# Kernel tuning notes

Measured on AMD Instinct MI355X. Metric: run time of the kernel, lower is better.

Reference implementation:

```python
import jax, jax.numpy as jnp
import numpy as np

B, T, D, H, WIN, G = 2, 2048, 768, 12, 16, 32
HD = D // H            # 64
K = 2 * WIN + 1        # local kernel size = 33


def setup_inputs() -> dict:
    key = jax.random.key(0)
    ks = jax.random.split(key, 5)
    s = 1.0 / np.sqrt(D).astype(np.float32)
    x = jax.random.normal(ks[0], (B, T, D), jnp.float32)
    # first G tokens of every batch are global (matches original's nonzero(global_mask[b]))
    global_mask = jnp.zeros((B, T), jnp.int32).at[:, :G].set(1)
    Wq = jax.random.normal(ks[1], (D, D), jnp.float32) * s
    Wk = jax.random.normal(ks[2], (D, D), jnp.float32) * s
    Wv = jax.random.normal(ks[3], (D, D), jnp.float32) * s
    Wo = jax.random.normal(ks[4], (D, D), jnp.float32) * s
    bq = jnp.zeros((D,), jnp.float32)
    bk = jnp.zeros((D,), jnp.float32)
    bv = jnp.zeros((D,), jnp.float32)
    bo = jnp.zeros((D,), jnp.float32)
    return {"x": x, "global_mask": global_mask, "Wq": Wq, "bq": bq,
            "Wk": Wk, "bk": bk, "Wv": Wv, "bv": bv, "Wo": Wo, "bo": bo}


def reference(x, global_mask, Wq, bq, Wk, bk, Wv, bv, Wo, bo):
    def split_heads(y):
        return y.reshape(B, T, H, HD).transpose(0, 2, 1, 3)  # [B,H,T,HD]

    q = split_heads(x @ Wq + bq)
    k = split_heads(x @ Wk + bk)
    v = split_heads(x @ Wv + bv)

    scale = 1.0 / np.sqrt(HD).astype(np.float32)

    offs = jnp.arange(-WIN, WIN + 1)
    idx = jnp.arange(T)[:, None] + offs[None, :]          # [T,K]
    valid = (idx >= 0) & (idx < T)                        # [T,K]
    idxc = jnp.clip(idx, 0, T - 1)

    k_loc = k[:, :, idxc]                                 # [B,H,T,K,HD]
    s_loc = jnp.einsum('bhtd,bhtkd->bhtk', q, k_loc) * scale
    s_loc = jnp.where(valid, s_loc, -jnp.inf)             # out-of-range excluded from softmax

    # global tokens (same positions for every batch by construction)
    g_idx = jnp.nonzero(global_mask[0], size=G)[0]        # [G]
    k_g = k[:, :, g_idx]                                  # [B,H,G,HD]
    v_g = v[:, :, g_idx]
    s_g = jnp.einsum('bhtd,bhgd->bhtg', q, k_g) * scale   # [B,H,T,G]

    # joint softmax over [local window, global tokens] (globals in window are double-counted,
    # exactly as in the original torch.cat([local_s, g_score]))
    attn = jax.nn.softmax(jnp.concatenate([s_loc, s_g], axis=-1), axis=-1)
    a_loc = jnp.where(valid, attn[..., :K], 0.0)          # [B,H,T,K]
    a_g = attn[..., K:]                                   # [B,H,T,G]

    v_loc = v[:, :, idxc]                                 # [B,H,T,K,HD]
    ctx = (jnp.einsum('bhtk,bhtkd->bhtd', a_loc, v_loc)
           + jnp.einsum('bhtg,bhgd->bhtd', a_g, v_g))     # [B,H,T,HD]

    out = ctx.transpose(0, 2, 1, 3).reshape(B, T, D) @ Wo + bo

    # dense attention map: scatter local band (add; invalid entries are 0),
    # then overwrite global columns (matches original write order)
    rows = jnp.arange(T)[:, None]                         # [T,1]
    full_attn = jnp.zeros((B, H, T, T), jnp.float32)
    full_attn = full_attn.at[:, :, rows, idxc].add(a_loc)
    full_attn = full_attn.at[:, :, :, g_idx].set(a_g)
    return out, full_attn
```

## Files before the change

kernel.cpp:

```cpp
#include <hip/hip_runtime.h>

typedef unsigned short u16;
typedef __attribute__((ext_vector_type(4))) u16 u16x4;
typedef __attribute__((ext_vector_type(8))) u16 u16x8;
typedef __attribute__((ext_vector_type(8))) short bf16x8;
typedef __attribute__((ext_vector_type(4))) float f32x4;

#define BB 2
#define TT 2048
#define DD 768
#define NH 12
#define HDIM 64
#define NQKV 2304
#define MM 4096

__device__ __forceinline__ u16 f2bf(float f) {
  unsigned u = __float_as_uint(f);
  u += 0x7fffu + ((u >> 16) & 1u);
  return (u16)(u >> 16);
}
__device__ __forceinline__ float bf2f(u16 s) {
  return __uint_as_float(((unsigned)s) << 16);
}
__device__ __forceinline__ void async_load16(const void* g, void* l) {
  __builtin_amdgcn_global_load_lds((const __attribute__((address_space(1))) void*)g,
                                   (__attribute__((address_space(3))) void*)l, 16, 0, 0);
}

__global__ __launch_bounds__(256) void prep_all(const float* __restrict__ x,
                                                const float* __restrict__ Wq, const float* __restrict__ Wk,
                                                const float* __restrict__ Wv, const float* __restrict__ Wo,
                                                const int* __restrict__ gm,
                                                const float* __restrict__ bq, const float* __restrict__ bk,
                                                const float* __restrict__ bv,
                                                u16* __restrict__ xb, u16* __restrict__ wqkvT,
                                                u16* __restrict__ woT,
                                                int* __restrict__ gidx, float* __restrict__ biasqkv) {
  __shared__ float tile[32][33];
  const int bid = blockIdx.x;
  const int tid = threadIdx.x;
  if (bid < 3072) {
    int i = bid * 256 + tid;
    float4 v = ((const float4*)x)[i];
    u16x4 o = { f2bf(v.x), f2bf(v.y), f2bf(v.z), f2bf(v.w) };
    ((u16x4*)xb)[i] = o;
  } else if (bid < 5376) {
    int r = bid - 3072;
    int z = r / 576; r %= 576;
    int kx = r % 24, ny = r / 24;
    const float* W = (z == 0) ? Wq : (z == 1) ? Wk : (z == 2) ? Wv : Wo;
    u16* dst = (z < 3) ? (wqkvT + (size_t)z * DD * DD) : woT;
    int k0 = kx * 32, n0 = ny * 32;
    int tx = tid & 31, ty = tid >> 5;
#pragma unroll
    for (int j = 0; j < 4; ++j)
      tile[ty + j * 8][tx] = W[(size_t)(k0 + ty + j * 8) * DD + n0 + tx];
    __syncthreads();
#pragma unroll
    for (int j = 0; j < 4; ++j)
      dst[(size_t)(n0 + ty + j * 8) * DD + k0 + tx] = f2bf(tile[tx][ty + j * 8]);
  } else {
    for (int n = tid; n < NQKV; n += 256)
      biasqkv[n] = (n < 768) ? bq[n] : (n < 1536) ? bk[n - 768] : bv[n - 1536];
    if (tid < 64) {
      int lane = tid;
      if (lane < 32) gidx[lane] = 0;
      int base = 0;
      for (int c0 = 0; c0 < TT; c0 += 64) {
        int mval = gm[c0 + lane];
        unsigned long long bal = __ballot(mval != 0);
        int pre = __popcll(bal & ((1ull << lane) - 1ull));
        if (mval && (base + pre) < 32) gidx[base + pre] = c0 + lane;
        base += __popcll(bal);
        if (base >= 32) break;
      }
    }
  }
}

__global__ __launch_bounds__(256) void gemm_qkv(const u16* __restrict__ A, const u16* __restrict__ BT,
                                                const float* __restrict__ bias, u16* __restrict__ C,
                                                int Ndim, int Kd) {
  __shared__ __attribute__((aligned(16))) u16 As[128 * 64];
  __shared__ __attribute__((aligned(16))) u16 Bs[128 * 64];
  const int tid = threadIdx.x;
  const int wave = tid >> 6, lane = tid & 63;
  const int m0 = blockIdx.x * 128, n0 = blockIdx.y * 128;
  const int wm = (wave & 1) << 6, wn = (wave >> 1) << 6;
  const int lr = lane & 15, lk = lane >> 4;
  const int srow_b = lane >> 3;
  const int scol = (lane & 7) * 8;

  f32x4 acc[4][4] = {};

  const int kIters = Kd >> 6;
  for (int kt = 0; kt < kIters; ++kt) {
#pragma unroll
    for (int cc = 0; cc < 4; ++cc) {
      int c = wave * 4 + cc;
      int srow = c * 8 + srow_b;
      async_load16(A + (size_t)(m0 + srow) * Kd + (kt << 6) + scol, (void*)(As + c * 512));
      async_load16(BT + (size_t)(n0 + srow) * Kd + (kt << 6) + scol, (void*)(Bs + c * 512));
    }
    __syncthreads();
#pragma unroll
    for (int kc = 0; kc < 2; ++kc) {
      bf16x8 af[4], bfr[4];
#pragma unroll
      for (int i = 0; i < 4; ++i)
        af[i] = *(const bf16x8*)(As + (wm + i * 16 + lr) * 64 + kc * 32 + lk * 8);
#pragma unroll
      for (int j = 0; j < 4; ++j)
        bfr[j] = *(const bf16x8*)(Bs + (wn + j * 16 + lr) * 64 + kc * 32 + lk * 8);
#pragma unroll
      for (int i = 0; i < 4; ++i)
#pragma unroll
        for (int j = 0; j < 4; ++j)
          acc[i][j] = __builtin_amdgcn_mfma_f32_16x16x32_bf16(af[i], bfr[j], acc[i][j], 0, 0, 0);
    }
    __syncthreads();
  }

#pragma unroll
  for (int i = 0; i < 4; ++i) {
    const int row = m0 + wm + i * 16 + lk * 4;
#pragma unroll
    for (int j = 0; j < 4; ++j) {
      const int col = n0 + wn + j * 16 + lr;
      const float bs = bias[col];
#pragma unroll
      for (int r = 0; r < 4; ++r)
        C[(size_t)(row + r) * Ndim + col] = f2bf(acc[i][j][r] + bs);
    }
  }
}

__global__ __launch_bounds__(256) void attn_kernel(const u16* __restrict__ qb,
                                                   const int* __restrict__ gidx,
                                                   u16* __restrict__ ctxb,
                                                   float* __restrict__ probsG) {
  __shared__ __attribute__((aligned(16))) u16 Kl[96 * 72];
  __shared__ __attribute__((aligned(16))) u16 Kg[32 * 72];
  __shared__ __attribute__((aligned(16))) u16 Vl[96 * 72];
  __shared__ __attribute__((aligned(16))) u16 Vg[32 * 72];
  __shared__ __attribute__((aligned(16))) float probs[64 * 68];

  const int tid = threadIdx.x;
  const int blk = blockIdx.x;
  const int chunk = blk & 31;
  const int h = (blk >> 5) % NH;
  const int b = blk / 384;
  const int t0 = chunk << 6;

  {
    const int r = tid >> 3;
    const int c8 = (tid & 7) << 3;
#pragma unroll
    for (int it = 0; it < 3; ++it) {
      int rr = it * 32 + r;
      int t = t0 - 16 + rr;
      t = t < 0 ? 0 : (t > TT - 1 ? TT - 1 : t);
      const u16* src = qb + (size_t)(b * TT + t) * NQKV + h * HDIM + c8;
      *(u16x8*)(Kl + rr * 72 + c8) = *(const u16x8*)(src + 768);
      *(u16x8*)(Vl + rr * 72 + c8) = *(const u16x8*)(src + 1536);
    }
    {
      int t = gidx[r];
      const u16* src = qb + (size_t)(b * TT + t) * NQKV + h * HDIM + c8;
      *(u16x8*)(Kg + r * 72 + c8) = *(const u16x8*)(src + 768);
      *(u16x8*)(Vg + r * 72 + c8) = *(const u16x8*)(src + 1536);
    }
  }
  __syncthreads();

  const int tl = tid >> 2, sub = tid & 3;
  const int t = t0 + tl;
  const u16* qp = qb + (size_t)(b * TT + t) * NQKV + h * HDIM;
  u16x8 qpk[8];
#pragma unroll
  for (int i = 0; i < 8; ++i) qpk[i] = *(const u16x8*)(qp + i * 8);

  float sc[17];
  float mmax = -__builtin_inff();
#pragma unroll
  for (int i = 0; i < 17; ++i) {
    const int s = sub + (i << 2);
    const u16* kp;
    bool valid;
    if (s < 33) { kp = Kl + (tl + s) * 72; int j = t - 16 + s; valid = (j >= 0) && (j < TT); }
    else if (s < 65) { kp = Kg + (s - 33) * 72; valid = true; }
    else { kp = Kg; valid = false; }
    float d = 0.f;
#pragma unroll
    for (int i2 = 0; i2 < 8; ++i2) {
      u16x8 kv = *(const u16x8*)(kp + i2 * 8);
      u16x8 qq = qpk[i2];
#pragma unroll
      for (int e = 0; e < 8; ++e) d += bf2f(qq[e]) * bf2f(kv[e]);
    }
    sc[i] = valid ? d * 0.125f : -__builtin_inff();
    mmax = fmaxf(mmax, sc[i]);
  }
  mmax = fmaxf(mmax, __shfl_xor(mmax, 1));
  mmax = fmaxf(mmax, __shfl_xor(mmax, 2));
  float sum = 0.f;
#pragma unroll
  for (int i = 0; i < 17; ++i) { sc[i] = __expf(sc[i] - mmax); sum += sc[i]; }
  sum += __shfl_xor(sum, 1);
  sum += __shfl_xor(sum, 2);
  const float inv = 1.0f / sum;
#pragma unroll
  for (int i = 0; i < 17; ++i) {
    const int s = sub + (i << 2);
    sc[i] *= inv;
    if (s < 65) probs[tl * 68 + s] = sc[i];
  }
  __syncthreads();

  float cacc[16];
#pragma unroll
  for (int i = 0; i < 16; ++i) cacc[i] = 0.f;
#pragma unroll 1
  for (int k = 0; k < 65; ++k) {
    const float pv = probs[tl * 68 + k];
    const u16* vp = (k < 33) ? (Vl + (tl + k) * 72) : (Vg + (k - 33) * 72);
    const u16* vq = vp + (sub << 4);
    u16x8 v0 = *(const u16x8*)(vq);
    u16x8 v1 = *(const u16x8*)(vq + 8);
#pragma unroll
    for (int e = 0; e < 8; ++e) { cacc[e] += pv * bf2f(v0[e]); cacc[8 + e] += pv * bf2f(v1[e]); }
  }
  {
    u16x8 cb0, cb1;
#pragma unroll
    for (int e = 0; e < 8; ++e) { cb0[e] = f2bf(cacc[e]); cb1[e] = f2bf(cacc[8 + e]); }
    u16* dst = ctxb + (size_t)(b * TT + t) * DD + h * HDIM + (sub << 4);
    *(u16x8*)dst = cb0;
    *(u16x8*)(dst + 8) = cb1;
  }

  {
    float4* dst = (float4*)(probsG + ((size_t)(b * NH + h) * TT + t0) * 68);
    const float4* srcp = (const float4*)probs;
#pragma unroll 1
    for (int i = tid; i < 1088; i += 256) dst[i] = srcp[i];
  }
}

#define G2_BLOCKS 384
__global__ __launch_bounds__(256) void tail_k(const u16* __restrict__ ctxb, const u16* __restrict__ woT,
                                              const float* __restrict__ bo, float* __restrict__ out,
                                              const float* __restrict__ probsG, const int* __restrict__ gidx,
                                              float* __restrict__ fattn) {
  __shared__ __attribute__((aligned(16))) u16 sA[64 * 64];
  __shared__ __attribute__((aligned(16))) u16 sB[128 * 64];
  const int tid = threadIdx.x;
  const int bid = blockIdx.x;

  if (bid < G2_BLOCKS) {
    const int wave = tid >> 6, lane = tid & 63;
    const int m0 = (bid & 63) * 64, n0 = (bid >> 6) * 128;
    const int wn = wave << 5;
    const int lr = lane & 15, lk = lane >> 4;
    const int srow_b = lane >> 3;
    const int scol = (lane & 7) * 8;

    f32x4 acc[4][2] = {};
    for (int kt = 0; kt < DD / 64; ++kt) {
#pragma unroll
      for (int cc = 0; cc < 2; ++cc) {
        int c = wave * 2 + cc;
        int srow = c * 8 + srow_b;
        async_load16(ctxb + (size_t)(m0 + srow) * DD + (kt << 6) + scol, (void*)(sA + c * 512));
      }
#pragma unroll
      for (int cc = 0; cc < 4; ++cc) {
        int c = wave * 4 + cc;
        int srow = c * 8 + srow_b;
        async_load16(woT + (size_t)(n0 + srow) * DD + (kt << 6) + scol, (void*)(sB + c * 512));
      }
      __syncthreads();
#pragma unroll
      for (int kc = 0; kc < 2; ++kc) {
        bf16x8 af[4], bfr[2];
#pragma unroll
        for (int i = 0; i < 4; ++i)
          af[i] = *(const bf16x8*)(sA + (i * 16 + lr) * 64 + kc * 32 + lk * 8);
#pragma unroll
        for (int j = 0; j < 2; ++j)
          bfr[j] = *(const bf16x8*)(sB + (wn + j * 16 + lr) * 64 + kc * 32 + lk * 8);
#pragma unroll
        for (int i = 0; i < 4; ++i)
#pragma unroll
          for (int j = 0; j < 2; ++j)
            acc[i][j] = __builtin_amdgcn_mfma_f32_16x16x32_bf16(af[i], bfr[j], acc[i][j], 0, 0, 0);
      }
      __syncthreads();
    }
#pragma unroll
    for (int i = 0; i < 4; ++i) {
      const int row = m0 + i * 16 + lk * 4;
#pragma unroll
      for (int j = 0; j < 2; ++j) {
        const int col = n0 + wn + j * 16 + lr;
        const float bs = bo[col];
#pragma unroll
        for (int r = 0; r < 4; ++r)
          out[(size_t)(row + r) * DD + col] = acc[i][j][r] + bs;
      }
    }
  } else {
    float* Lp = (float*)sA;
    int* gidxs = (int*)sB;
    const int fid = bid - G2_BLOCKS;
    const int slice = fid & 127;
    const int h = (fid >> 7) % NH;
    const int b = fid / (128 * NH);
    const int t0s = slice << 4;

    const float4* src = (const float4*)(probsG + ((size_t)(b * NH + h) * TT + t0s) * 68);
    for (int i = tid; i < 272; i += 256) ((float4*)Lp)[i] = src[i];
    if (tid < 32) gidxs[tid] = gidx[tid];
    __syncthreads();

    float* fbase = fattn + ((size_t)(b * NH + h) * TT + t0s) * TT;
#pragma unroll 1
    for (int it = 0; it < 32; ++it) {
      int q = it * 256 + tid;
      int rl = q >> 9;
      int c4 = (q & 511) << 2;
      int trow = t0s + rl;
      float4 v = make_float4(0.f, 0.f, 0.f, 0.f);
      int kk = c4 - trow + 16;
      if (kk >= -3 && kk < 33) {
        float* vp = &v.x;
#pragma unroll
        for (int e = 0; e < 4; ++e) {
          int k2 = kk + e;
          if ((unsigned)k2 < 33u) vp[e] = Lp[rl * 68 + k2];
        }
      }
      *(float4*)(fbase + (size_t)rl * TT + c4) = v;
    }
    __syncthreads();
#pragma unroll
    for (int rep = 0; rep < 2; ++rep) {
      int w = rep * 256 + tid;
      int rl = w >> 5, g = w & 31;
      fbase[(size_t)rl * TT + gidxs[g]] = Lp[rl * 68 + 33 + g];
    }
  }
}

extern "C" void kernel_launch(void* const* d_in, const int* in_sizes, int n_in,
                              void* d_out, int out_size, void* d_ws, size_t ws_size,
                              hipStream_t stream) {
  const float* x  = (const float*)d_in[0];
  const int* gm   = (const int*)d_in[1];
  const float* Wq = (const float*)d_in[2];
  const float* bq = (const float*)d_in[3];
  const float* Wk = (const float*)d_in[4];
  const float* bk = (const float*)d_in[5];
  const float* Wv = (const float*)d_in[6];
  const float* bv = (const float*)d_in[7];
  const float* Wo = (const float*)d_in[8];
  const float* bo = (const float*)d_in[9];

  float* out = (float*)d_out;
  float* fattn = out + (size_t)BB * TT * DD;

  char* p = (char*)d_ws;
  u16* xb      = (u16*)p;  p += (size_t)MM * DD * 2;
  u16* wqkvT   = (u16*)p;  p += (size_t)NQKV * DD * 2;
  u16* woT     = (u16*)p;  p += (size_t)DD * DD * 2;
  float* biasq = (float*)p; p += (size_t)NQKV * 4;
  int* gidx    = (int*)p;  p += 128;
  u16* qkvb    = (u16*)p;  p += (size_t)MM * NQKV * 2;
  u16* ctxb    = (u16*)p;  p += (size_t)MM * DD * 2;
  float* probsG= (float*)p; p += (size_t)MM * NH * 68 * 4;

  prep_all<<<5377, 256, 0, stream>>>(x, Wq, Wk, Wv, Wo, gm, bq, bk, bv,
                                     xb, wqkvT, woT, gidx, biasq);
  gemm_qkv<<<dim3(MM / 128, NQKV / 128), 256, 0, stream>>>(xb, wqkvT, biasq, qkvb, NQKV, DD);
  attn_kernel<<<BB * NH * (TT / 64), 256, 0, stream>>>(qkvb, gidx, ctxb, probsG);
  tail_k<<<G2_BLOCKS + BB * NH * (TT / 16), 256, 0, stream>>>(ctxb, woT, bo, out, probsG, gidx, fattn);
}
```

Measured before the change: 537.4 us.

## Write dense attention map directly from attention kernel, drop probs staging buffer

The attention kernel now writes the full dense T×T probability rows itself, using nontemporal stores from its shared-memory probs tile. This removes the probsG round trip and the separate fill blocks in the tail kernel, which becomes a plain output GEMM. The trade-off is that the large 400MB-class write now sits inside attn_kernel's 768 blocks instead of being spread over many small blocks, so store throughput per block and occupancy decide the outcome. The probs row pitch also changes from 68 to 66.

Result: no change. 533.0 us (-0.8%).

```diff
diff --git a/kernel.cpp b/kernel.cpp
--- a/kernel.cpp
+++ b/kernel.cpp
@@ -138,12 +138,13 @@
 __global__ __launch_bounds__(256) void attn_kernel(const u16* __restrict__ qb,
                                                    const int* __restrict__ gidx,
                                                    u16* __restrict__ ctxb,
-                                                   float* __restrict__ probsG) {
+                                                   float* __restrict__ fattn) {
   __shared__ __attribute__((aligned(16))) u16 Kl[96 * 72];
   __shared__ __attribute__((aligned(16))) u16 Kg[32 * 72];
   __shared__ __attribute__((aligned(16))) u16 Vl[96 * 72];
   __shared__ __attribute__((aligned(16))) u16 Vg[32 * 72];
-  __shared__ __attribute__((aligned(16))) float probs[64 * 68];
+  __shared__ __attribute__((aligned(16))) float probs[64 * 66];
+  __shared__ int gidxs[32];
 
   const int tid = threadIdx.x;
   const int blk = blockIdx.x;
@@ -170,6 +171,7 @@
       *(u16x8*)(Kg + r * 72 + c8) = *(const u16x8*)(src + 768);
       *(u16x8*)(Vg + r * 72 + c8) = *(const u16x8*)(src + 1536);
     }
+    if (tid < 32) gidxs[tid] = gidx[tid];
   }
   __syncthreads();
 
@@ -213,7 +215,7 @@
   for (int i = 0; i < 17; ++i) {
     const int s = sub + (i << 2);
     sc[i] *= inv;
-    if (s < 65) probs[tl * 68 + s] = sc[i];
+    if (s < 65) probs[tl * 66 + s] = sc[i];
   }
   __syncthreads();
 
@@ -222,7 +224,7 @@
   for (int i = 0; i < 16; ++i) cacc[i] = 0.f;
 #pragma unroll 1
   for (int k = 0; k < 65; ++k) {
-    const float pv = probs[tl * 68 + k];
+    const float pv = probs[tl * 66 + k];
     const u16* vp = (k < 33) ? (Vl + (tl + k) * 72) : (Vg + (k - 33) * 72);
     const u16* vq = vp + (sub << 4);
     u16x8 v0 = *(const u16x8*)(vq);
@@ -239,115 +241,88 @@
     *(u16x8*)(dst + 8) = cb1;
   }
 
-  {
-    float4* dst = (float4*)(probsG + ((size_t)(b * NH + h) * TT + t0) * 68);
-    const float4* srcp = (const float4*)probs;
-#pragma unroll 1
-    for (int i = tid; i < 1088; i += 256) dst[i] = srcp[i];
-  }
-}
-
-#define G2_BLOCKS 384
-__global__ __launch_bounds__(256) void tail_k(const u16* __restrict__ ctxb, const u16* __restrict__ woT,
-                                              const float* __restrict__ bo, float* __restrict__ out,
-                                              const float* __restrict__ probsG, const int* __restrict__ gidx,
-                                              float* __restrict__ fattn) {
+  float* fbase = fattn + ((size_t)(b * NH + h) * TT + t0) * TT;
+#pragma unroll 2
+  for (int it = 0; it < 128; ++it) {
+    int q = it * 256 + tid;
+    int rl = q >> 9;
+    int c4 = (q & 511) << 2;
+    int trow = t0 + rl;
+    f32x4 v = {0.f, 0.f, 0.f, 0.f};
+    int kk = c4 - trow + 16;
+    if (kk >= -3 && kk < 33) {
+#pragma unroll
+      for (int e = 0; e < 4; ++e) {
+        int k2 = kk + e;
+        if ((unsigned)k2 < 33u) v[e] = probs[rl * 66 + k2];
+      }
+    }
+    __builtin_nontemporal_store(v, (f32x4*)(fbase + (size_t)rl * TT + c4));
+  }
+  __syncthreads();
+#pragma unroll
+  for (int rep = 0; rep < 8; ++rep) {
+    int w = rep * 256 + tid;
+    int rl = w >> 5, g = w & 31;
+    fbase[(size_t)rl * TT + gidxs[g]] = probs[rl * 66 + 33 + g];
+  }
+}
+
+__global__ __launch_bounds__(256) void gemm_out(const u16* __restrict__ ctxb, const u16* __restrict__ woT,
+                                                const float* __restrict__ bo, float* __restrict__ out) {
   __shared__ __attribute__((aligned(16))) u16 sA[64 * 64];
   __shared__ __attribute__((aligned(16))) u16 sB[128 * 64];
   const int tid = threadIdx.x;
   const int bid = blockIdx.x;
-
-  if (bid < G2_BLOCKS) {
-    const int wave = tid >> 6, lane = tid & 63;
-    const int m0 = (bid & 63) * 64, n0 = (bid >> 6) * 128;
-    const int wn = wave << 5;
-    const int lr = lane & 15, lk = lane >> 4;
-    const int srow_b = lane >> 3;
-    const int scol = (lane & 7) * 8;
-
-    f32x4 acc[4][2] = {};
-    for (int kt = 0; kt < DD / 64; ++kt) {
-#pragma unroll
-      for (int cc = 0; cc < 2; ++cc) {
-        int c = wave * 2 + cc;
-        int srow = c * 8 + srow_b;
-        async_load16(ctxb + (size_t)(m0 + srow) * DD + (kt << 6) + scol, (void*)(sA + c * 512));
-      }
-#pragma unroll
-      for (int cc = 0; cc < 4; ++cc) {
-        int c = wave * 4 + cc;
-        int srow = c * 8 + srow_b;
-        async_load16(woT + (size_t)(n0 + srow) * DD + (kt << 6) + scol, (void*)(sB + c * 512));
-      }
-      __syncthreads();
-#pragma unroll
-      for (int kc = 0; kc < 2; ++kc) {
-        bf16x8 af[4], bfr[2];
-#pragma unroll
-        for (int i = 0; i < 4; ++i)
-          af[i] = *(const bf16x8*)(sA + (i * 16 + lr) * 64 + kc * 32 + lk * 8);
+  const int wave = tid >> 6, lane = tid & 63;
+  const int m0 = (bid & 63) * 64, n0 = (bid >> 6) * 128;
+  const int wn = wave << 5;
+  const int lr = lane & 15, lk = lane >> 4;
+  const int srow_b = lane >> 3;
+  const int scol = (lane & 7) * 8;
+
+  f32x4 acc[4][2] = {};
+  for (int kt = 0; kt < DD / 64; ++kt) {
+#pragma unroll
+    for (int cc = 0; cc < 2; ++cc) {
+      int c = wave * 2 + cc;
+      int srow = c * 8 + srow_b;
+      async_load16(ctxb + (size_t)(m0 + srow) * DD + (kt << 6) + scol, (void*)(sA + c * 512));
+    }
+#pragma unroll
+    for (int cc = 0; cc < 4; ++cc) {
+      int c = wave * 4 + cc;
+      int srow = c * 8 + srow_b;
+      async_load16(woT + (size_t)(n0 + srow) * DD + (kt << 6) + scol, (void*)(sB + c * 512));
+    }
+    __syncthreads();
+#pragma unroll
+    for (int kc = 0; kc < 2; ++kc) {
+      bf16x8 af[4], bfr[2];
+#pragma unroll
+      for (int i = 0; i < 4; ++i)
+        af[i] = *(const bf16x8*)(sA + (i * 16 + lr) * 64 + kc * 32 + lk * 8);
+#pragma unroll
+      for (int j = 0; j < 2; ++j)
+        bfr[j] = *(const bf16x8*)(sB + (wn + j * 16 + lr) * 64 + kc * 32 + lk * 8);
+#pragma unroll
+      for (int i = 0; i < 4; ++i)
 #pragma unroll
         for (int j = 0; j < 2; ++j)
-          bfr[j] = *(const bf16x8*)(sB + (wn + j * 16 + lr) * 64 + kc * 32 + lk * 8);
-#pragma unroll
-        for (int i = 0; i < 4; ++i)
-#pragma unroll
-          for (int j = 0; j < 2; ++j)
-            acc[i][j] = __builtin_amdgcn_mfma_f32_16x16x32_bf16(af[i], bfr[j], acc[i][j], 0, 0, 0);
-      }
-      __syncthreads();
-    }
-#pragma unroll
-    for (int i = 0; i < 4; ++i) {
-      const int row = m0 + i * 16 + lk * 4;
-#pragma unroll
-      for (int j = 0; j < 2; ++j) {
-        const int col = n0 + wn + j * 16 + lr;
-        const float bs = bo[col];
-#pragma unroll
-        for (int r = 0; r < 4; ++r)
-          out[(size_t)(row + r) * DD + col] = acc[i][j][r] + bs;
-      }
-    }
-  } else {
-    float* Lp = (float*)sA;
-    int* gidxs = (int*)sB;
-    const int fid = bid - G2_BLOCKS;
-    const int slice = fid & 127;
-    const int h = (fid >> 7) % NH;
-    const int b = fid / (128 * NH);
-    const int t0s = slice << 4;
-
-    const float4* src = (const float4*)(probsG + ((size_t)(b * NH + h) * TT + t0s) * 68);
-    for (int i = tid; i < 272; i += 256) ((float4*)Lp)[i] = src[i];
-    if (tid < 32) gidxs[tid] = gidx[tid];
-    __syncthreads();
-
-    float* fbase = fattn + ((size_t)(b * NH + h) * TT + t0s) * TT;
-#pragma unroll 1
-    for (int it = 0; it < 32; ++it) {
-      int q = it * 256 + tid;
-      int rl = q >> 9;
-      int c4 = (q & 511) << 2;
-      int trow = t0s + rl;
-      float4 v = make_float4(0.f, 0.f, 0.f, 0.f);
-      int kk = c4 - trow + 16;
-      if (kk >= -3 && kk < 33) {
-        float* vp = &v.x;
-#pragma unroll
-        for (int e = 0; e < 4; ++e) {
-          int k2 = kk + e;
-          if ((unsigned)k2 < 33u) vp[e] = Lp[rl * 68 + k2];
-        }
-      }
-      *(float4*)(fbase + (size_t)rl * TT + c4) = v;
-    }
-    __syncthreads();
-#pragma unroll
-    for (int rep = 0; rep < 2; ++rep) {
-      int w = rep * 256 + tid;
-      int rl = w >> 5, g = w & 31;
-      fbase[(size_t)rl * TT + gidxs[g]] = Lp[rl * 68 + 33 + g];
+          acc[i][j] = __builtin_amdgcn_mfma_f32_16x16x32_bf16(af[i], bfr[j], acc[i][j], 0, 0, 0);
+    }
+    __syncthreads();
+  }
+#pragma unroll
+  for (int i = 0; i < 4; ++i) {
+    const int row = m0 + i * 16 + lk * 4;
+#pragma unroll
+    for (int j = 0; j < 2; ++j) {
+      const int col = n0 + wn + j * 16 + lr;
+      const float bs = bo[col];
+#pragma unroll
+      for (int r = 0; r < 4; ++r)
+        out[(size_t)(row + r) * DD + col] = acc[i][j][r] + bs;
     }
   }
 }
@@ -377,11 +352,10 @@
   int* gidx    = (int*)p;  p += 128;
   u16* qkvb    = (u16*)p;  p += (size_t)MM * NQKV * 2;
   u16* ctxb    = (u16*)p;  p += (size_t)MM * DD * 2;
-  float* probsG= (float*)p; p += (size_t)MM * NH * 68 * 4;
 
   prep_all<<<5377, 256, 0, stream>>>(x, Wq, Wk, Wv, Wo, gm, bq, bk, bv,
                                      xb, wqkvT, woT, gidx, biasq);
   gemm_qkv<<<dim3(MM / 128, NQKV / 128), 256, 0, stream>>>(xb, wqkvT, biasq, qkvb, NQKV, DD);
-  attn_kernel<<<BB * NH * (TT / 64), 256, 0, stream>>>(qkvb, gidx, ctxb, probsG);
-  tail_k<<<G2_BLOCKS + BB * NH * (TT / 16), 256, 0, stream>>>(ctxb, woT, bo, out, probsG, gidx, fattn);
-}
+  attn_kernel<<<BB * NH * (TT / 64), 256, 0, stream>>>(qkvb, gidx, ctxb, fattn);
+  gemm_out<<<384, 256, 0, stream>>>(ctxb, woT, bo, out);
+}
```
